# Kernel tuning notes

Measured on AMD Instinct MI355X. Metric: run time of the kernel, lower is better.

## Reference

```python
import jax, jax.numpy as jnp
import numpy as np

B, N, C, H = 8192, 17, 512, 8
HD = C // H  # head dim = 64


def setup_inputs() -> dict:
    key = jax.random.key(0)
    ks = jax.random.split(key, 7)
    s = 0.02
    return {
        "x": jax.random.normal(ks[0], (B, N, C), dtype=jnp.float32),
        "W_qkv": jax.random.normal(ks[1], (C, 3 * C), dtype=jnp.float32) * s,
        "b_qkv": jax.random.normal(ks[2], (3 * C,), dtype=jnp.float32) * s,
        "outer": jax.random.normal(ks[3], (H, N, N), dtype=jnp.float32) * s,
        "alpha": jnp.ones((1,), dtype=jnp.float32),
        "W_proj": jax.random.normal(ks[4], (C, C), dtype=jnp.float32) * s,
        "b_proj": jax.random.normal(ks[5], (C,), dtype=jnp.float32) * s,
    }


def reference(x, W_qkv, b_qkv, outer, alpha, W_proj, b_proj):
    scale = HD ** -0.5
    qkv = x @ W_qkv + b_qkv                       # [B,N,3C]
    qkv = qkv.reshape(B, N, 3, H, HD)
    q = jnp.transpose(qkv[:, :, 0], (0, 2, 1, 3))  # [B,H,N,HD]
    k = jnp.transpose(qkv[:, :, 1], (0, 2, 1, 3))
    v = jnp.transpose(qkv[:, :, 2], (0, 2, 1, 3))
    # comb=False path: (q @ k^T + alpha * outer) * scale, softmax, @ v
    logits = (jnp.einsum('bhnd,bhmd->bhnm', q, k) + alpha * outer[None]) * scale
    attn = jax.nn.softmax(logits, axis=-1)        # [B,H,N,N]
    out = jnp.einsum('bhnm,bhmd->bhnd', attn, v)  # [B,H,N,HD]
    out = jnp.transpose(out, (0, 2, 1, 3)).reshape(B, N, C)
    return out @ W_proj + b_proj
```

## Files before the change

### kernel.cpp

```cpp
#include <hip/hip_runtime.h>
#include <stdint.h>


typedef __attribute__((ext_vector_type(4))) float f32x4;
typedef _Float16 f16x8 __attribute__((ext_vector_type(8)));
typedef _Float16 f16x2 __attribute__((ext_vector_type(2)));

__device__ __forceinline__ unsigned short f2h(float f) {
  return __builtin_bit_cast(unsigned short, (_Float16)f);
}
__device__ __forceinline__ float h2f(unsigned short h) {
  return (float)__builtin_bit_cast(_Float16, h);
}
__device__ __forceinline__ float fdot2u(uint32_t a, uint32_t b, float c) {
  return __builtin_amdgcn_fdot2(__builtin_bit_cast(f16x2, a),
                                __builtin_bit_cast(f16x2, b), c, false);
}

#define GLOAD_LDS16(gptr, lptr)                                          \
  __builtin_amdgcn_global_load_lds(                                      \
      (__attribute__((address_space(1))) void*)(gptr),                   \
      (__attribute__((address_space(3))) void*)(lptr), 16, 0, 0)

__device__ __forceinline__ f32x4 mfma16(f16x8 a, f16x8 b, f32x4 c) {
  return __builtin_amdgcn_mfma_f32_16x16x32_f16(a, b, c, 0, 0, 0);
}

__global__ __launch_bounds__(256) void k_cvt(const float* __restrict__ in,
                                             unsigned short* __restrict__ out,
                                             long n4) {
  long i = (long)blockIdx.x * 256 + threadIdx.x;
  if (i >= n4) return;
  float4 a = reinterpret_cast<const float4*>(in)[i];
  ushort4 o;
  o.x = f2h(a.x); o.y = f2h(a.y); o.z = f2h(a.z); o.w = f2h(a.w);
  reinterpret_cast<ushort4*>(out)[i] = o;
}

template <bool PERM>
__global__ __launch_bounds__(256) void k_cvt_t(const float* __restrict__ W,
                                               unsigned short* __restrict__ Wt,
                                               int K, int Norig) {
  int i = blockIdx.x * 256 + threadIdx.x;
  if (i >= K * Norig) return;
  int np = i / K, k = i - np * K;
  int n = np;
  if (PERM) {
    int h = np / 192, rem = np - h * 192;
    int t = rem >> 6, d = rem & 63;
    n = t * 512 + h * 64 + d;
  }
  Wt[i] = f2h(W[(size_t)k * Norig + n]);
}

__global__ __launch_bounds__(256) void k_permb(const float* __restrict__ b,
                                               float* __restrict__ bqp) {
  int np = blockIdx.x * 256 + threadIdx.x;
  if (np >= 1536) return;
  int h = np / 192, rem = np - h * 192;
  int t = rem >> 6, d = rem & 63;
  bqp[np] = b[t * 512 + h * 64 + d];
}

#define FBUF 20480

__global__ __launch_bounds__(512, 4) void k_fused(
    const unsigned short* __restrict__ A,
    const unsigned short* __restrict__ Bt,
    const float* __restrict__ bqp,
    const float* __restrict__ outer,
    const float* __restrict__ alpha_p,
    unsigned short* __restrict__ ao) {
  __shared__ __align__(16) unsigned short smem[2 * FBUF];

  const int tid = threadIdx.x;
  const int w = tid >> 6, lane = tid & 63;
  const int wm = w >> 2, wn = w & 3;
  const int lr = lane & 15, lk = lane >> 4;

  const int bid = (blockIdx.x & 7) * ((int)gridDim.x >> 3) + (blockIdx.x >> 3);
  const int mt = bid >> 3, h = bid & 7;
  const int batch0 = mt * 7;
  const int brow = batch0 * 17;
  const int bcol = h * 192;

  const int srowl = lane >> 3;
  const int scol = ((lane & 7) ^ srowl) << 3;

  f32x4 acc[4][3];
#pragma unroll
  for (int m = 0; m < 4; m++)
#pragma unroll
    for (int n = 0; n < 3; n++) acc[m][n] = f32x4{0.f, 0.f, 0.f, 0.f};

  auto STAGE = [&](int t, int buf) {
    unsigned short* dstbase = smem + buf * FBUF;
#pragma unroll
    for (int s5 = 0; s5 < 5; ++s5) {
      const int s = w + s5 * 8;
      unsigned short* dst = dstbase + s * 512;
      const unsigned short* src;
      if (s < 16) {
        int gr = brow + s * 8 + srowl;
        if (gr > 139263) gr = 139263;
        src = A + (size_t)gr * 512 + t * 64 + scol;
      } else {
        int r = (s - 16) * 8 + srowl;
        src = Bt + (size_t)(bcol + r) * 512 + t * 64 + scol;
      }
      GLOAD_LDS16(src, dst);
    }
  };

  STAGE(0, 0);
  asm volatile("s_waitcnt vmcnt(0)" ::: "memory");
  __builtin_amdgcn_s_barrier();

  for (int t = 0; t < 8; ++t) {
    const int ub = (t & 1) * FBUF;
    if (t < 7) STAGE(t + 1, (t + 1) & 1);
    const unsigned short* sa = smem + ub + (wm * 64 + lr) * 64;
    const unsigned short* sb = smem + ub + 8192 + (wn * 48 + lr) * 64;
#pragma unroll
    for (int kk = 0; kk < 2; ++kk) {
      const int gx = (((kk << 2) + lk) ^ (lr & 7)) << 3;
      f16x8 av0 = *(const f16x8*)(sa + gx);
      f16x8 av1 = *(const f16x8*)(sa + 1024 + gx);
      f16x8 av2 = *(const f16x8*)(sa + 2048 + gx);
      f16x8 av3 = *(const f16x8*)(sa + 3072 + gx);
      f16x8 bv0 = *(const f16x8*)(sb + gx);
      f16x8 bv1 = *(const f16x8*)(sb + 1024 + gx);
      f16x8 bv2 = *(const f16x8*)(sb + 2048 + gx);
      acc[0][0] = mfma16(av0, bv0, acc[0][0]);
      acc[0][1] = mfma16(av0, bv1, acc[0][1]);
      acc[0][2] = mfma16(av0, bv2, acc[0][2]);
      acc[1][0] = mfma16(av1, bv0, acc[1][0]);
      acc[1][1] = mfma16(av1, bv1, acc[1][1]);
      acc[1][2] = mfma16(av1, bv2, acc[1][2]);
      acc[2][0] = mfma16(av2, bv0, acc[2][0]);
      acc[2][1] = mfma16(av2, bv1, acc[2][1]);
      acc[2][2] = mfma16(av2, bv2, acc[2][2]);
      acc[3][0] = mfma16(av3, bv0, acc[3][0]);
      acc[3][1] = mfma16(av3, bv1, acc[3][1]);
      acc[3][2] = mfma16(av3, bv2, acc[3][2]);
    }
    asm volatile("s_waitcnt vmcnt(0)" ::: "memory");
    __builtin_amdgcn_s_barrier();
  }

  float* s_attn = (float*)(smem + 25600);
  float* s_inv = (float*)(smem + 25600 + 2 * (7 * 17 * 18));

  {
    const int er0 = wm * 64 + (lane >> 4) * 4;
    const int ec0 = wn * 48 + lr;
    float bvv[3];
#pragma unroll
    for (int nf = 0; nf < 3; ++nf) bvv[nf] = bqp[bcol + ec0 + nf * 16];
#pragma unroll
    for (int mf = 0; mf < 4; ++mf)
#pragma unroll
      for (int nf = 0; nf < 3; ++nf)
#pragma unroll
        for (int rr = 0; rr < 4; ++rr)
          smem[(er0 + mf * 16 + rr) * 200 + ec0 + nf * 16] =
              f2h(acc[mf][nf][rr] + bvv[nf]);
  }
  __syncthreads();

  const int nb = min(7, 8192 - batch0);
  if (w < nb) {
    const float alpha = alpha_p[0];
    const unsigned short* sA0 = smem + (w * 17) * 200;
    for (int p = lane; p < 289; p += 64) {
      const int r = p / 17, m = p - r * 17;
      const uint4* qr = (const uint4*)(sA0 + r * 200);
      const uint4* km = (const uint4*)(sA0 + m * 200 + 64);
      float s = 0.f;
#pragma unroll
      for (int c = 0; c < 8; ++c) {
        uint4 qa = qr[c], ka = km[c];
        s = fdot2u(qa.x, ka.x, s);
        s = fdot2u(qa.y, ka.y, s);
        s = fdot2u(qa.z, ka.z, s);
        s = fdot2u(qa.w, ka.w, s);
      }
      s_attn[(w * 17 + r) * 18 + m] = (s + alpha * outer[h * 289 + p]) * 0.125f;
    }
    __builtin_amdgcn_wave_barrier();
    asm volatile("" ::: "memory");

    if (lane < 17) {
      float mx = -1e30f;
#pragma unroll
      for (int m = 0; m < 17; m++)
        mx = fmaxf(mx, s_attn[(w * 17 + lane) * 18 + m]);
      float s = 0.f;
#pragma unroll
      for (int m = 0; m < 17; m++) {
        float e = __expf(s_attn[(w * 17 + lane) * 18 + m] - mx);
        s_attn[(w * 17 + lane) * 18 + m] = e;
        s += e;
      }
      s_inv[w * 17 + lane] = 1.f / s;
    }
    __builtin_amdgcn_wave_barrier();
    asm volatile("" ::: "memory");

    float vr[17];
#pragma unroll
    for (int m = 0; m < 17; m++)
      vr[m] = h2f(smem[(w * 17 + m) * 200 + 128 + lane]);
    const size_t obase = ((size_t)(batch0 + w) * 17) * 512 + h * 64 + lane;
#pragma unroll 1
    for (int r = 0; r < 17; ++r) {
      float o = 0.f;
#pragma unroll
      for (int m = 0; m < 17; m++) o += s_attn[(w * 17 + r) * 18 + m] * vr[m];
      ao[obase + (size_t)r * 512] = f2h(o * s_inv[w * 17 + r]);
    }
  }
}

#define PBUF 16384

__global__ __launch_bounds__(512, 4) void k_proj(
    const unsigned short* __restrict__ A,
    const unsigned short* __restrict__ Bt,
    const float* __restrict__ bias,
    float* __restrict__ C) {
  __shared__ __align__(16) unsigned short smem[2 * PBUF];

  const int tid = threadIdx.x;
  const int w = tid >> 6, lane = tid & 63;
  const int wm = w >> 2, wn = w & 3;
  const int lr = lane & 15, lk = lane >> 4;

  const int bid = (blockIdx.x & 7) * ((int)gridDim.x >> 3) + (blockIdx.x >> 3);
  const int brow = (bid >> 2) << 7;
  const int bcol = (bid & 3) << 7;

  const int srowl = lane >> 3;
  const int scol = ((lane & 7) ^ srowl) << 3;

  f32x4 acc[4][2];
#pragma unroll
  for (int m = 0; m < 4; m++)
#pragma unroll
    for (int n = 0; n < 2; n++) acc[m][n] = f32x4{0.f, 0.f, 0.f, 0.f};

  auto STAGE = [&](int t, int buf) {
    unsigned short* dstbase = smem + buf * PBUF;
#pragma unroll
    for (int s4 = 0; s4 < 4; ++s4) {
      const int s = w + s4 * 8;
      unsigned short* dst = dstbase + s * 512;
      const unsigned short* src =
          (s < 16) ? A + (size_t)(brow + s * 8 + srowl) * 512 + t * 64 + scol
                   : Bt + (size_t)(bcol + (s - 16) * 8 + srowl) * 512 + t * 64 + scol;
      GLOAD_LDS16(src, dst);
    }
  };

  STAGE(0, 0);
  asm volatile("s_waitcnt vmcnt(0)" ::: "memory");
  __builtin_amdgcn_s_barrier();

  for (int t = 0; t < 8; ++t) {
    const int ub = (t & 1) * PBUF;
    if (t < 7) STAGE(t + 1, (t + 1) & 1);
    const unsigned short* sa = smem + ub + (wm * 64 + lr) * 64;
    const unsigned short* sb = smem + ub + 8192 + (wn * 32 + lr) * 64;
#pragma unroll
    for (int kk = 0; kk < 2; ++kk) {
      const int gx = (((kk << 2) + lk) ^ (lr & 7)) << 3;
      f16x8 av0 = *(const f16x8*)(sa + gx);
      f16x8 av1 = *(const f16x8*)(sa + 1024 + gx);
      f16x8 av2 = *(const f16x8*)(sa + 2048 + gx);
      f16x8 av3 = *(const f16x8*)(sa + 3072 + gx);
      f16x8 bv0 = *(const f16x8*)(sb + gx);
      f16x8 bv1 = *(const f16x8*)(sb + 1024 + gx);
      acc[0][0] = mfma16(av0, bv0, acc[0][0]);
      acc[0][1] = mfma16(av0, bv1, acc[0][1]);
      acc[1][0] = mfma16(av1, bv0, acc[1][0]);
      acc[1][1] = mfma16(av1, bv1, acc[1][1]);
      acc[2][0] = mfma16(av2, bv0, acc[2][0]);
      acc[2][1] = mfma16(av2, bv1, acc[2][1]);
      acc[3][0] = mfma16(av3, bv0, acc[3][0]);
      acc[3][1] = mfma16(av3, bv1, acc[3][1]);
    }
    asm volatile("s_waitcnt vmcnt(0)" ::: "memory");
    __builtin_amdgcn_s_barrier();
  }

  const int orow = brow + wm * 64 + (lane >> 4) * 4;
  const int ocol0 = bcol + wn * 32 + lr;
#pragma unroll
  for (int n = 0; n < 2; n++) {
    const int col = ocol0 + n * 16;
    const float bv = bias[col];
#pragma unroll
    for (int m = 0; m < 4; m++) {
      const int row = orow + m * 16;
#pragma unroll
      for (int r = 0; r < 4; r++)
        C[(size_t)(row + r) * 512 + col] = acc[m][n][r] + bv;
    }
  }
}

extern "C" void kernel_launch(void* const* d_in, const int* in_sizes, int n_in,
                              void* d_out, int out_size, void* d_ws,
                              size_t ws_size, hipStream_t stream) {
  const float* x      = (const float*)d_in[0];
  const float* W_qkv  = (const float*)d_in[1];
  const float* b_qkv  = (const float*)d_in[2];
  const float* outer  = (const float*)d_in[3];
  const float* alpha  = (const float*)d_in[4];
  const float* W_proj = (const float*)d_in[5];
  const float* b_proj = (const float*)d_in[6];

  char* ws = (char*)d_ws;
  unsigned short* xb  = (unsigned short*)(ws);
  unsigned short* ao  = (unsigned short*)(ws + 142606336);
  unsigned short* wqt = (unsigned short*)(ws + 285212672);
  unsigned short* wpt = (unsigned short*)(ws + 286785536);
  float*          bqp = (float*)(ws + 287309824);

  k_cvt<<<dim3(69632), dim3(256), 0, stream>>>(x, xb, 17825792L);
  k_cvt_t<true><<<dim3(3072), dim3(256), 0, stream>>>(W_qkv, wqt, 512, 1536);
  k_cvt_t<false><<<dim3(1024), dim3(256), 0, stream>>>(W_proj, wpt, 512, 512);
  k_permb<<<dim3(6), dim3(256), 0, stream>>>(b_qkv, bqp);

  k_fused<<<dim3(9368), dim3(512), 0, stream>>>(xb, wqt, bqp, outer, alpha, ao);

  k_proj<<<dim3(4352), dim3(512), 0, stream>>>(ao, wpt, b_proj, (float*)d_out);
}
```

Measured before the change: 594.0 us.

## Compute per-head attention with MFMA tiles and V-transposed LDS layout

Replaces the scalar fdot2 QK^T and scalar PV loops in the fused attention epilogue with 16x16 MFMA tiles. Row 16 and column 16 are handled separately with dot products. Q/K are stored in a padded row layout and V is stored transposed per batch in LDS so it can feed MFMA B operands. Softmax now uses cross-lane shuffles instead of a single-lane serial loop. This adds handling for the seventeenth row and column and a new LDS layout, which could cost more LDS traffic and bank conflicts.

```diff
diff --git a/kernel.cpp b/kernel.cpp
--- a/kernel.cpp
+++ b/kernel.cpp
@@ -63,6 +63,10 @@
 }
 
 #define FBUF 20480
+#define SQ_OFF 0
+#define VT_OFF 17408
+#define PL_OFF 33792
+#define SE_OFF 38912
 
 __global__ __launch_bounds__(512, 4) void k_fused(
     const unsigned short* __restrict__ A,
@@ -148,76 +152,144 @@
     __builtin_amdgcn_s_barrier();
   }
 
-  float* s_attn = (float*)(smem + 25600);
-  float* s_inv = (float*)(smem + 25600 + 2 * (7 * 17 * 18));
-
+  unsigned short* SQ = smem + SQ_OFF;
+  unsigned short* VT = smem + VT_OFF;
+  unsigned short* PL = smem + PL_OFF;
+  float* SE = (float*)(smem + SE_OFF);
   {
     const int er0 = wm * 64 + (lane >> 4) * 4;
     const int ec0 = wn * 48 + lr;
-    float bvv[3];
-#pragma unroll
-    for (int nf = 0; nf < 3; ++nf) bvv[nf] = bqp[bcol + ec0 + nf * 16];
-#pragma unroll
-    for (int mf = 0; mf < 4; ++mf)
-#pragma unroll
-      for (int nf = 0; nf < 3; ++nf)
-#pragma unroll
-        for (int rr = 0; rr < 4; ++rr)
-          smem[(er0 + mf * 16 + rr) * 200 + ec0 + nf * 16] =
-              f2h(acc[mf][nf][rr] + bvv[nf]);
+#pragma unroll
+    for (int nf = 0; nf < 3; ++nf) {
+      const int col = ec0 + nf * 16;
+      const float bv = bqp[bcol + col];
+#pragma unroll
+      for (int mf = 0; mf < 4; ++mf) {
+        const int t0 = er0 + mf * 16;
+        float v0 = acc[mf][nf][0] + bv, v1 = acc[mf][nf][1] + bv;
+        float v2 = acc[mf][nf][2] + bv, v3 = acc[mf][nf][3] + bv;
+        if (col < 128) {
+          SQ[(t0 + 0) * 136 + col] = f2h(v0);
+          SQ[(t0 + 1) * 136 + col] = f2h(v1);
+          SQ[(t0 + 2) * 136 + col] = f2h(v2);
+          SQ[(t0 + 3) * 136 + col] = f2h(v3);
+        } else {
+          const int d = col - 128;
+#pragma unroll
+          for (int rr = 0; rr < 4; ++rr) {
+            const int tt = t0 + rr;
+            const int bb = tt / 17, tl = tt - bb * 17;
+            float vv = (rr == 0 ? v0 : rr == 1 ? v1 : rr == 2 ? v2 : v3);
+            if (bb < 7) VT[bb * 2048 + d * 32 + tl] = f2h(vv);
+          }
+        }
+      }
+    }
   }
   __syncthreads();
 
   const int nb = min(7, 8192 - batch0);
   if (w < nb) {
     const float alpha = alpha_p[0];
-    const unsigned short* sA0 = smem + (w * 17) * 200;
-    for (int p = lane; p < 289; p += 64) {
-      const int r = p / 17, m = p - r * 17;
-      const uint4* qr = (const uint4*)(sA0 + r * 200);
-      const uint4* km = (const uint4*)(sA0 + m * 200 + 64);
-      float s = 0.f;
+    const int base = w * 17;
+    unsigned short* PLw = PL + w * 640;
+    unsigned short* VTw = VT + w * 2048;
+    float* SEw = SE + w * 34;
+
+    for (int i = lane; i < 16 * 24; i += 64)
+      PLw[(i / 24) * 40 + 16 + (i % 24)] = 0;
+
+    f32x4 sAcc = f32x4{0.f, 0.f, 0.f, 0.f};
+#pragma unroll
+    for (int kk = 0; kk < 2; ++kk) {
+      f16x8 qa = *(const f16x8*)(SQ + (base + lr) * 136 + kk * 32 + lk * 8);
+      f16x8 kb = *(const f16x8*)(SQ + (base + lr) * 136 + 64 + kk * 32 + lk * 8);
+      sAcc = mfma16(qa, kb, sAcc);
+    }
+
+    if (lane < 33) {
+      const int r_ = (lane < 16) ? lane : 16;
+      const int m_ = (lane < 16) ? 16 : lane - 16;
+      const uint4* qr = (const uint4*)(SQ + (base + r_) * 136);
+      const uint4* kr = (const uint4*)(SQ + (base + m_) * 136 + 64);
+      float dt = 0.f;
 #pragma unroll
       for (int c = 0; c < 8; ++c) {
-        uint4 qa = qr[c], ka = km[c];
-        s = fdot2u(qa.x, ka.x, s);
-        s = fdot2u(qa.y, ka.y, s);
-        s = fdot2u(qa.z, ka.z, s);
-        s = fdot2u(qa.w, ka.w, s);
+        uint4 qa = qr[c], ka = kr[c];
+        dt = fdot2u(qa.x, ka.x, dt);
+        dt = fdot2u(qa.y, ka.y, dt);
+        dt = fdot2u(qa.z, ka.z, dt);
+        dt = fdot2u(qa.w, ka.w, dt);
       }
-      s_attn[(w * 17 + r) * 18 + m] = (s + alpha * outer[h * 289 + p]) * 0.125f;
+      float sv = (dt + alpha * outer[h * 289 + r_ * 17 + m_]) * 0.125f;
+      SEw[(lane < 16) ? lane : (17 + m_)] = sv;
     }
     __builtin_amdgcn_wave_barrier();
     asm volatile("" ::: "memory");
 
-    if (lane < 17) {
-      float mx = -1e30f;
-#pragma unroll
-      for (int m = 0; m < 17; m++)
-        mx = fmaxf(mx, s_attn[(w * 17 + lane) * 18 + m]);
-      float s = 0.f;
-#pragma unroll
-      for (int m = 0; m < 17; m++) {
-        float e = __expf(s_attn[(w * 17 + lane) * 18 + m] - mx);
-        s_attn[(w * 17 + lane) * 18 + m] = e;
-        s += e;
-      }
-      s_inv[w * 17 + lane] = 1.f / s;
-    }
+    const int g4 = (lane >> 4) * 4;
+    float sp[4], rmax[4], p[4], pe[4], rsum[4], inv[4];
+#pragma unroll
+    for (int j = 0; j < 4; ++j) {
+      sp[j] = (sAcc[j] + alpha * outer[h * 289 + (g4 + j) * 17 + lr]) * 0.125f;
+      rmax[j] = sp[j];
+    }
+#pragma unroll
+    for (int d = 1; d < 16; d <<= 1)
+#pragma unroll
+      for (int j = 0; j < 4; ++j)
+        rmax[j] = fmaxf(rmax[j], __shfl_xor(rmax[j], d));
+#pragma unroll
+    for (int j = 0; j < 4; ++j) {
+      float ec = SEw[g4 + j];
+      rmax[j] = fmaxf(rmax[j], ec);
+      p[j] = __expf(sp[j] - rmax[j]);
+      pe[j] = __expf(ec - rmax[j]);
+      rsum[j] = p[j];
+    }
+#pragma unroll
+    for (int d = 1; d < 16; d <<= 1)
+#pragma unroll
+      for (int j = 0; j < 4; ++j) rsum[j] += __shfl_xor(rsum[j], d);
+#pragma unroll
+    for (int j = 0; j < 4; ++j) {
+      rsum[j] += pe[j];
+      inv[j] = 1.f / rsum[j];
+      PLw[(g4 + j) * 40 + lr] = f2h(p[j]);
+    }
+    if (lr == 0)
+#pragma unroll
+      for (int j = 0; j < 4; ++j) PLw[(g4 + j) * 40 + 16] = f2h(pe[j]);
     __builtin_amdgcn_wave_barrier();
     asm volatile("" ::: "memory");
 
-    float vr[17];
-#pragma unroll
-    for (int m = 0; m < 17; m++)
-      vr[m] = h2f(smem[(w * 17 + m) * 200 + 128 + lane]);
-    const size_t obase = ((size_t)(batch0 + w) * 17) * 512 + h * 64 + lane;
+    f16x8 pa = *(const f16x8*)(PLw + lr * 40 + lk * 8);
+    f32x4 o[4];
+#pragma unroll
+    for (int nf = 0; nf < 4; ++nf) {
+      f16x8 vb = *(const f16x8*)(VTw + (nf * 16 + lr) * 32 + lk * 8);
+      o[nf] = mfma16(pa, vb, f32x4{0.f, 0.f, 0.f, 0.f});
+    }
+    const size_t gr0 = (size_t)(brow + base) * 512 + h * 64;
+#pragma unroll
+    for (int nf = 0; nf < 4; ++nf)
+#pragma unroll
+      for (int j = 0; j < 4; ++j)
+        ao[gr0 + (size_t)(g4 + j) * 512 + nf * 16 + lr] =
+            f2h(o[nf][j] * inv[j]);
+
+    {
+      float mx16 = -1e30f;
 #pragma unroll 1
-    for (int r = 0; r < 17; ++r) {
-      float o = 0.f;
-#pragma unroll
-      for (int m = 0; m < 17; m++) o += s_attn[(w * 17 + r) * 18 + m] * vr[m];
-      ao[obase + (size_t)r * 512] = f2h(o * s_inv[w * 17 + r]);
+      for (int m = 0; m < 17; ++m) mx16 = fmaxf(mx16, SEw[17 + m]);
+      float o16 = 0.f, s16 = 0.f;
+#pragma unroll 1
+      for (int m = 0; m < 17; ++m) {
+        float pm = __expf(SEw[17 + m] - mx16);
+        s16 += pm;
+        o16 += pm * h2f(VTw[lane * 32 + m]);
+      }
+      ao[gr0 + (size_t)16 * 512 + lane] = f2h(o16 / s16);
     }
   }
 }
```

New measurement: 597.3 us. No clear change (+0.5%).
